# Optimization experiments

Measured on AMD Instinct MI355X. Metric: run time of the kernel, lower is better.

The kernel has to match this reference:

```python
import jax, jax.numpy as jnp
import numpy as np

B, T = 64, 512
L, D = 2048, 512


def setup_inputs() -> dict:
    key = jax.random.key(0)
    k1, k2, k3 = jax.random.split(key, 3)
    label_sequences = jax.random.randint(k1, (B, T), 0, L)
    source_embeddings = jax.random.normal(k2, (L, D), dtype=jnp.float32)
    target_embeddings = jax.random.normal(k3, (L, D), dtype=jnp.float32)
    return {
        "label_sequences": label_sequences,
        "source_embeddings": source_embeddings,
        "target_embeddings": target_embeddings,
    }


def reference(label_sequences, source_embeddings, target_embeddings):
    # source_index = labels[:, :-1], target_index = labels[:, 1:]
    src_idx = label_sequences[:, :-1]          # [B, T-1]
    tgt_idx = label_sequences[:, 1:]           # [B, T-1]
    # Gather source embeddings per transition pair: [B, T-1, D]
    src = source_embeddings[src_idx]
    # Logits over all target labels: [B, T-1, L]
    logits = jnp.einsum("btd,ld->btl", src, target_embeddings)
    # Row-wise log_softmax over target labels (dim=1 in torch == last axis here)
    logp = jax.nn.log_softmax(logits, axis=-1)
    # Pick the actual next label's log-probability: [B, T-1]
    scores = jnp.take_along_axis(logp, tgt_idx[..., None], axis=-1)[..., 0]
    return scores
```

## Files before the change

kernel.cpp:

```cpp
#include <hip/hip_runtime.h>
#include <hip/hip_bf16.h>

#define L_CLS 2048
#define D_DIM 512
#define T_SZ  512
#define NT    511
#define NOUT  (64 * NT)
#define NCHUNK 32
#define LDSS  136
#define LOG2E 1.4426950408889634f
#define LN2   0.6931471805599453f
#define SHIFT 128.0f

typedef __attribute__((ext_vector_type(8)))  short bf16x8;
typedef __attribute__((ext_vector_type(4)))  float f32x4;
typedef __attribute__((ext_vector_type(16))) float f32x16;

static __device__ __forceinline__ short f2bf(float x) {
    return (short)__bfloat16_as_ushort(__float2bfloat16(x));
}

__global__ void conv_bf16(const float* __restrict__ srcE, const float* __restrict__ tgtE,
                          __hip_bfloat16* __restrict__ Sb, __hip_bfloat16* __restrict__ Tb) {
    int i = blockIdx.x * blockDim.x + threadIdx.x;
    if (i >= (L_CLS * D_DIM) / 8) return;
    const f32x4* s4 = reinterpret_cast<const f32x4*>(srcE) + i * 2;
    const f32x4* t4 = reinterpret_cast<const f32x4*>(tgtE) + i * 2;
    f32x4 s0 = s4[0], s1 = s4[1];
    f32x4 t0 = t4[0], t1 = t4[1];
    bf16x8 so, to;
#pragma unroll
    for (int j = 0; j < 4; ++j) {
        so[j] = f2bf(s0[j]); so[j + 4] = f2bf(s1[j]);
        to[j] = f2bf(t0[j]); to[j + 4] = f2bf(t1[j]);
    }
    reinterpret_cast<bf16x8*>(Sb)[i] = so;
    reinterpret_cast<bf16x8*>(Tb)[i] = to;
}

__launch_bounds__(512, 1)
__global__ void gemm_lse_bf16(const __hip_bfloat16* __restrict__ Sb,
                              const __hip_bfloat16* __restrict__ Tb,
                              float* __restrict__ psum,
                              float* __restrict__ M) {
    __shared__ __hip_bfloat16 Blds[2][128 * LDSS];

    const int tid  = threadIdx.x;
    const int wave = tid >> 6;
    const int lane = tid & 63;
    const int l31  = lane & 31;
    const int hk   = lane >> 5;
    const int rs   = (wave & 3) * 32;
    const int chf  = wave >> 2;
    const int C    = blockIdx.x * 128;
    const int Rb   = blockIdx.y * 128;
    const int Ar   = Rb + rs + l31;

    f32x16 acc0, acc1;
#pragma unroll
    for (int r = 0; r < 16; ++r) { acc0[r] = 0.f; acc1[r] = 0.f; }

    bf16x8 stg[4], an[8];
#pragma unroll
    for (int i = 0; i < 4; ++i) {
        int p = tid + 512 * i;
        stg[i] = *reinterpret_cast<const bf16x8*>(
            &Tb[(C + (p >> 4)) * D_DIM + (p & 15) * 8]);
    }
#pragma unroll
    for (int ks = 0; ks < 8; ++ks)
        an[ks] = *reinterpret_cast<const bf16x8*>(
            &Sb[Ar * D_DIM + ks * 16 + hk * 8]);
#pragma unroll
    for (int i = 0; i < 4; ++i) {
        int p = tid + 512 * i;
        *reinterpret_cast<bf16x8*>(&Blds[0][(p >> 4) * LDSS + (p & 15) * 8]) = stg[i];
    }
    __syncthreads();

#pragma unroll
    for (int s = 0; s < 4; ++s) {
        const int cur = s & 1;
        bf16x8 a[8];
#pragma unroll
        for (int ks = 0; ks < 8; ++ks) a[ks] = an[ks];

        if (s < 3) {
#pragma unroll
            for (int i = 0; i < 4; ++i) {
                int p = tid + 512 * i;
                stg[i] = *reinterpret_cast<const bf16x8*>(
                    &Tb[(C + (p >> 4)) * D_DIM + (s + 1) * 128 + (p & 15) * 8]);
            }
#pragma unroll
            for (int ks = 0; ks < 8; ++ks)
                an[ks] = *reinterpret_cast<const bf16x8*>(
                    &Sb[Ar * D_DIM + (s + 1) * 128 + ks * 16 + hk * 8]);
        }

        const __hip_bfloat16* Bb = Blds[cur];
#pragma unroll
        for (int ks = 0; ks < 8; ++ks) {
            const int off = ks * 16 + hk * 8;
            bf16x8 b0 = *reinterpret_cast<const bf16x8*>(&Bb[(chf * 64 + l31) * LDSS + off]);
            bf16x8 b1 = *reinterpret_cast<const bf16x8*>(&Bb[(chf * 64 + 32 + l31) * LDSS + off]);
            acc0 = __builtin_amdgcn_mfma_f32_32x32x16_bf16(a[ks], b0, acc0, 0, 0, 0);
            acc1 = __builtin_amdgcn_mfma_f32_32x32x16_bf16(a[ks], b1, acc1, 0, 0, 0);
        }

        if (s < 3) {
#pragma unroll
            for (int i = 0; i < 4; ++i) {
                int p = tid + 512 * i;
                *reinterpret_cast<bf16x8*>(
                    &Blds[cur ^ 1][(p >> 4) * LDSS + (p & 15) * 8]) = stg[i];
            }
            __syncthreads();
        }
    }

    float p[16];
#pragma unroll
    for (int r = 0; r < 16; ++r) {
        int grow = Rb + rs + (r & 3) + 8 * (r >> 2) + 4 * hk;
        size_t base = (size_t)grow * L_CLS + C + chf * 64 + l31;
        M[base]      = acc0[r];
        M[base + 32] = acc1[r];
        p[r] = exp2f(acc0[r] * LOG2E - SHIFT) + exp2f(acc1[r] * LOG2E - SHIFT);
    }
#pragma unroll
    for (int off = 1; off < 32; off <<= 1)
#pragma unroll
        for (int r = 0; r < 16; ++r) p[r] += __shfl_xor(p[r], off);
    if (l31 == 0) {
#pragma unroll
        for (int r = 0; r < 16; ++r) {
            int grow = Rb + rs + (r & 3) + 8 * (r >> 2) + 4 * hk;
            psum[grow * NCHUNK + blockIdx.x * 2 + chf] = p[r];
        }
    }
}

__launch_bounds__(256)
__global__ void scores_gather(const int* __restrict__ labels,
                              const float* __restrict__ psum,
                              const float* __restrict__ M,
                              float* __restrict__ out) {
    int o = blockIdx.x * 256 + threadIdx.x;
    if (o >= NOUT) return;
    int b = o / NT;
    int t = o - b * NT;
    int src = labels[b * T_SZ + t];
    int tgt = labels[b * T_SZ + t + 1];

    const f32x4* pv = reinterpret_cast<const f32x4*>(psum + src * NCHUNK);
    f32x4 sv = pv[0];
#pragma unroll
    for (int c = 1; c < NCHUNK / 4; ++c) {
        f32x4 v = pv[c];
        sv[0] += v[0]; sv[1] += v[1]; sv[2] += v[2]; sv[3] += v[3];
    }
    float S = (sv[0] + sv[1]) + (sv[2] + sv[3]);
    float lse = (log2f(S) + SHIFT) * LN2;
    out[o] = M[(size_t)src * L_CLS + tgt] - lse;
}

extern "C" void kernel_launch(void* const* d_in, const int* in_sizes, int n_in,
                              void* d_out, int out_size, void* d_ws, size_t ws_size,
                              hipStream_t stream) {
    const int*   labels = (const int*)d_in[0];
    const float* srcE   = (const float*)d_in[1];
    const float* tgtE   = (const float*)d_in[2];
    float*       out    = (float*)d_out;

    const size_t tbl = (size_t)L_CLS * D_DIM;
    __hip_bfloat16* Sb = (__hip_bfloat16*)d_ws;
    __hip_bfloat16* Tb = Sb + tbl;
    float* psum = (float*)((char*)d_ws + 2 * tbl * sizeof(__hip_bfloat16));
    float* M    = psum + (size_t)L_CLS * NCHUNK;

    conv_bf16<<<(int)(tbl / 8 + 255) / 256, 256, 0, stream>>>(srcE, tgtE, Sb, Tb);
    gemm_lse_bf16<<<dim3(16, 16), 512, 0, stream>>>(Sb, Tb, psum, M);
    scores_gather<<<(NOUT + 255) / 256, 256, 0, stream>>>(labels, psum, M, out);
}
```

Baseline: 29.74 us.

## Switch GEMM to 16x16x32 MFMA, single LDS buffer, and separate LSE kernel

```diff
diff --git a/kernel.cpp b/kernel.cpp
--- a/kernel.cpp
+++ b/kernel.cpp
@@ -12,9 +12,8 @@
 #define LN2   0.6931471805599453f
 #define SHIFT 128.0f
 
-typedef __attribute__((ext_vector_type(8)))  short bf16x8;
-typedef __attribute__((ext_vector_type(4)))  float f32x4;
-typedef __attribute__((ext_vector_type(16))) float f32x16;
+typedef __attribute__((ext_vector_type(8))) short bf16x8;
+typedef __attribute__((ext_vector_type(4))) float f32x4;
 
 static __device__ __forceinline__ short f2bf(float x) {
     return (short)__bfloat16_as_ushort(__float2bfloat16(x));
@@ -43,24 +42,26 @@
                               const __hip_bfloat16* __restrict__ Tb,
                               float* __restrict__ psum,
                               float* __restrict__ M) {
-    __shared__ __hip_bfloat16 Blds[2][128 * LDSS];
+    __shared__ __hip_bfloat16 Blds[128 * LDSS];
 
     const int tid  = threadIdx.x;
     const int wave = tid >> 6;
     const int lane = tid & 63;
-    const int l31  = lane & 31;
-    const int hk   = lane >> 5;
+    const int lr   = lane & 15;
+    const int hi   = lane >> 4;
     const int rs   = (wave & 3) * 32;
     const int chf  = wave >> 2;
     const int C    = blockIdx.x * 128;
     const int Rb   = blockIdx.y * 128;
-    const int Ar   = Rb + rs + l31;
+    const int R0   = Rb + rs;
 
-    f32x16 acc0, acc1;
+    f32x4 acc[2][4];
 #pragma unroll
-    for (int r = 0; r < 16; ++r) { acc0[r] = 0.f; acc1[r] = 0.f; }
+    for (int rf = 0; rf < 2; ++rf)
+#pragma unroll
+        for (int ct = 0; ct < 4; ++ct) acc[rf][ct] = (f32x4){0.f, 0.f, 0.f, 0.f};
 
-    bf16x8 stg[4], an[8];
+    bf16x8 stg[4], an[2][4];
 #pragma unroll
     for (int i = 0; i < 4; ++i) {
         int p = tid + 512 * i;
@@ -68,22 +69,25 @@
             &Tb[(C + (p >> 4)) * D_DIM + (p & 15) * 8]);
     }
 #pragma unroll
-    for (int ks = 0; ks < 8; ++ks)
-        an[ks] = *reinterpret_cast<const bf16x8*>(
-            &Sb[Ar * D_DIM + ks * 16 + hk * 8]);
+    for (int rf = 0; rf < 2; ++rf)
 #pragma unroll
-    for (int i = 0; i < 4; ++i) {
-        int p = tid + 512 * i;
-        *reinterpret_cast<bf16x8*>(&Blds[0][(p >> 4) * LDSS + (p & 15) * 8]) = stg[i];
-    }
-    __syncthreads();
+        for (int ks = 0; ks < 4; ++ks)
+            an[rf][ks] = *reinterpret_cast<const bf16x8*>(
+                &Sb[(R0 + rf * 16 + lr) * D_DIM + ks * 32 + hi * 8]);
 
+#pragma unroll 1
+    for (int s = 0; s < 4; ++s) {
 #pragma unroll
-    for (int s = 0; s < 4; ++s) {
-        const int cur = s & 1;
-        bf16x8 a[8];
+        for (int i = 0; i < 4; ++i) {
+            int p = tid + 512 * i;
+            *reinterpret_cast<bf16x8*>(&Blds[(p >> 4) * LDSS + (p & 15) * 8]) = stg[i];
+        }
+        bf16x8 a[2][4];
 #pragma unroll
-        for (int ks = 0; ks < 8; ++ks) a[ks] = an[ks];
+        for (int rf = 0; rf < 2; ++rf)
+#pragma unroll
+            for (int ks = 0; ks < 4; ++ks) a[rf][ks] = an[rf][ks];
+        __syncthreads();
 
         if (s < 3) {
 #pragma unroll
@@ -93,57 +97,72 @@
                     &Tb[(C + (p >> 4)) * D_DIM + (s + 1) * 128 + (p & 15) * 8]);
             }
 #pragma unroll
-            for (int ks = 0; ks < 8; ++ks)
-                an[ks] = *reinterpret_cast<const bf16x8*>(
-                    &Sb[Ar * D_DIM + (s + 1) * 128 + ks * 16 + hk * 8]);
+            for (int rf = 0; rf < 2; ++rf)
+#pragma unroll
+                for (int ks = 0; ks < 4; ++ks)
+                    an[rf][ks] = *reinterpret_cast<const bf16x8*>(
+                        &Sb[(R0 + rf * 16 + lr) * D_DIM + (s + 1) * 128 + ks * 32 + hi * 8]);
         }
 
-        const __hip_bfloat16* Bb = Blds[cur];
 #pragma unroll
-        for (int ks = 0; ks < 8; ++ks) {
-            const int off = ks * 16 + hk * 8;
-            bf16x8 b0 = *reinterpret_cast<const bf16x8*>(&Bb[(chf * 64 + l31) * LDSS + off]);
-            bf16x8 b1 = *reinterpret_cast<const bf16x8*>(&Bb[(chf * 64 + 32 + l31) * LDSS + off]);
-            acc0 = __builtin_amdgcn_mfma_f32_32x32x16_bf16(a[ks], b0, acc0, 0, 0, 0);
-            acc1 = __builtin_amdgcn_mfma_f32_32x32x16_bf16(a[ks], b1, acc1, 0, 0, 0);
+        for (int ks = 0; ks < 4; ++ks) {
+            const int off = ks * 32 + hi * 8;
+#pragma unroll
+            for (int ct = 0; ct < 4; ++ct) {
+                bf16x8 b = *reinterpret_cast<const bf16x8*>(
+                    &Blds[(chf * 64 + ct * 16 + lr) * LDSS + off]);
+                acc[0][ct] = __builtin_amdgcn_mfma_f32_16x16x32_bf16(a[0][ks], b, acc[0][ct], 0, 0, 0);
+                acc[1][ct] = __builtin_amdgcn_mfma_f32_16x16x32_bf16(a[1][ks], b, acc[1][ct], 0, 0, 0);
+            }
         }
+        __syncthreads();
+    }
 
-        if (s < 3) {
+#pragma unroll
+    for (int rf = 0; rf < 2; ++rf) {
+        float p[4];
+#pragma unroll
+        for (int i = 0; i < 4; ++i) {
+            int grow = R0 + rf * 16 + hi * 4 + i;
+            size_t base = (size_t)grow * L_CLS + C + chf * 64 + lr;
+            p[i] = 0.f;
+#pragma unroll
+            for (int ct = 0; ct < 4; ++ct) {
+                M[base + ct * 16] = acc[rf][ct][i];
+                p[i] += exp2f(acc[rf][ct][i] * LOG2E - SHIFT);
+            }
+        }
+#pragma unroll
+        for (int off = 1; off < 16; off <<= 1)
+#pragma unroll
+            for (int i = 0; i < 4; ++i) p[i] += __shfl_xor(p[i], off);
+        if (lr == 0) {
 #pragma unroll
             for (int i = 0; i < 4; ++i) {
-                int p = tid + 512 * i;
-                *reinterpret_cast<bf16x8*>(
-                    &Blds[cur ^ 1][(p >> 4) * LDSS + (p & 15) * 8]) = stg[i];
+                int grow = R0 + rf * 16 + hi * 4 + i;
+                psum[grow * NCHUNK + blockIdx.x * 2 + chf] = p[i];
             }
-            __syncthreads();
-        }
-    }
-
-    float p[16];
-#pragma unroll
-    for (int r = 0; r < 16; ++r) {
-        int grow = Rb + rs + (r & 3) + 8 * (r >> 2) + 4 * hk;
-        size_t base = (size_t)grow * L_CLS + C + chf * 64 + l31;
-        M[base]      = acc0[r];
-        M[base + 32] = acc1[r];
-        p[r] = exp2f(acc0[r] * LOG2E - SHIFT) + exp2f(acc1[r] * LOG2E - SHIFT);
-    }
-#pragma unroll
-    for (int off = 1; off < 32; off <<= 1)
-#pragma unroll
-        for (int r = 0; r < 16; ++r) p[r] += __shfl_xor(p[r], off);
-    if (l31 == 0) {
-#pragma unroll
-        for (int r = 0; r < 16; ++r) {
-            int grow = Rb + rs + (r & 3) + 8 * (r >> 2) + 4 * hk;
-            psum[grow * NCHUNK + blockIdx.x * 2 + chf] = p[r];
         }
     }
 }
 
+__global__ void lse_final(const float* __restrict__ psum, float* __restrict__ lse) {
+    int row = blockIdx.x * blockDim.x + threadIdx.x;
+    if (row >= L_CLS) return;
+    const f32x4* pv = reinterpret_cast<const f32x4*>(psum + row * NCHUNK);
+    f32x4 sv = pv[0];
+#pragma unroll
+    for (int c = 1; c < NCHUNK / 4; ++c) {
+        f32x4 v = pv[c];
+        sv[0] += v[0]; sv[1] += v[1]; sv[2] += v[2]; sv[3] += v[3];
+    }
+    float S = (sv[0] + sv[1]) + (sv[2] + sv[3]);
+    lse[row] = (log2f(S) + SHIFT) * LN2;
+}
+
 __launch_bounds__(256)
 __global__ void scores_gather(const int* __restrict__ labels,
-                              const float* __restrict__ psum,
+                              const float* __restrict__ lse,
                               const float* __restrict__ M,
                               float* __restrict__ out) {
     int o = blockIdx.x * 256 + threadIdx.x;
@@ -152,17 +171,7 @@
     int t = o - b * NT;
     int src = labels[b * T_SZ + t];
     int tgt = labels[b * T_SZ + t + 1];
-
-    const f32x4* pv = reinterpret_cast<const f32x4*>(psum + src * NCHUNK);
-    f32x4 sv = pv[0];
-#pragma unroll
-    for (int c = 1; c < NCHUNK / 4; ++c) {
-        f32x4 v = pv[c];
-        sv[0] += v[0]; sv[1] += v[1]; sv[2] += v[2]; sv[3] += v[3];
-    }
-    float S = (sv[0] + sv[1]) + (sv[2] + sv[3]);
-    float lse = (log2f(S) + SHIFT) * LN2;
-    out[o] = M[(size_t)src * L_CLS + tgt] - lse;
+    out[o] = M[(size_t)src * L_CLS + tgt] - lse[src];
 }
 
 extern "C" void kernel_launch(void* const* d_in, const int* in_sizes, int n_in,
@@ -177,9 +186,11 @@
     __hip_bfloat16* Sb = (__hip_bfloat16*)d_ws;
     __hip_bfloat16* Tb = Sb + tbl;
     float* psum = (float*)((char*)d_ws + 2 * tbl * sizeof(__hip_bfloat16));
-    float* M    = psum + (size_t)L_CLS * NCHUNK;
+    float* lse  = psum + (size_t)L_CLS * NCHUNK;
+    float* M    = lse + L_CLS;
 
     conv_bf16<<<(int)(tbl / 8 + 255) / 256, 256, 0, stream>>>(srcE, tgtE, Sb, Tb);
     gemm_lse_bf16<<<dim3(16, 16), 512, 0, stream>>>(Sb, Tb, psum, M);
-    scores_gather<<<(NOUT + 255) / 256, 256, 0, stream>>>(labels, psum, M, out);
+    lse_final<<<(L_CLS + 255) / 256, 256, 0, stream>>>(psum, lse);
+    scores_gather<<<(NOUT + 255) / 256, 256, 0, stream>>>(labels, lse, M, out);
 }
```

Result: slower. 31.17 us (+4.8%).
